# Kernel tuning notes

Measured on AMD Instinct MI355X. Metric: run time of the kernel, lower is better.

## Reference

```python
import jax, jax.numpy as jnp
import numpy as np

H = 8
D_MODEL = 512
NEG = -1e9  # fp32 masking value from the torch source


def setup_inputs() -> dict:
    key = jax.random.key(0)
    ks = jax.random.split(key, 13)
    B, T, C, D = 2, 512, 8, D_MODEL
    s = 1.0 / np.sqrt(D)
    inp = {
        "query": jax.random.normal(ks[0], (B, T, C, D), jnp.float32),
        "key": jax.random.normal(ks[1], (B, T, C, D), jnp.float32),
        "value": jax.random.normal(ks[2], (B, T, C, D), jnp.float32),
        "mask": jax.random.randint(ks[3], (B, T, T, 1), 0, 2, jnp.int32),
        # four Linear(d_model, d_model) layers, stored as (in, out)
        "Wq": jax.random.normal(ks[4], (D, D), jnp.float32) * s,
        "bq": jax.random.normal(ks[5], (D,), jnp.float32) * s,
        "Wk": jax.random.normal(ks[6], (D, D), jnp.float32) * s,
        "bk": jax.random.normal(ks[7], (D,), jnp.float32) * s,
        "Wv": jax.random.normal(ks[8], (D, D), jnp.float32) * s,
        "bv": jax.random.normal(ks[9], (D,), jnp.float32) * s,
        "Wo": jax.random.normal(ks[10], (D, D), jnp.float32) * s,
        "bo": jax.random.normal(ks[11], (D,), jnp.float32) * s,
    }
    return inp


def _mha(query, key, value, mask, Wq, bq, Wk, bk, Wv, bv, Wo, bo):
    B, T, C, D = query.shape
    h, dk = H, D // H

    def proj(x, W, b):
        y = (x @ W + b).reshape(B, T, C, h, dk)
        return jnp.transpose(y, (0, 3, 2, 1, 4))  # [B,h,C,T,dk] (torch transpose(1,3))

    q = proj(query, Wq, bq)
    k = proj(key, Wk, bk)
    v = proj(value, Wv, bv)

    scores = jnp.einsum("bhctd,bhcsd->bhcts", q, k) / np.sqrt(dk)  # [B,h,C,T,T]
    # The torch view/transpose/view dance is just a permutation putting C last;
    # it is equivalent to masking scores[b,h,c,t,s] where mask[b,t,s,0]==0
    # (mask broadcast over heads h and channels c).
    m = mask[:, :, :, 0]  # [B,T,Tk]
    scores = jnp.where(m[:, None, None, :, :] == 0, NEG, scores)
    p_attn = jax.nn.softmax(scores, axis=-1)
    # dropout omitted (inference/deterministic reference)
    x = jnp.einsum("bhcts,bhcsd->bhctd", p_attn, v)  # [B,h,C,T,dk]
    x = jnp.transpose(x, (0, 3, 2, 1, 4)).reshape(B, T, C, D)
    return x @ Wo + bo


def reference(query, key, value, mask, Wq, bq, Wk, bk, Wv, bv, Wo, bo):
    return _mha(query, key, value, mask, Wq, bq, Wk, bk, Wv, bv, Wo, bo)
```

## Files before the change

kernel.cpp:

```cpp
#include <hip/hip_runtime.h>
#include <hip/hip_bf16.h>

typedef __bf16 bf16;
typedef __bf16 bf16x8 __attribute__((ext_vector_type(8)));
typedef float floatx4 __attribute__((ext_vector_type(4)));


#define AS1 __attribute__((address_space(1)))
#define AS3 __attribute__((address_space(3)))

__device__ __forceinline__ void gload_lds16(const bf16* g, bf16* l) {
    __builtin_amdgcn_global_load_lds((const AS1 unsigned int*)g,
                                     (AS3 unsigned int*)l, 16, 0, 0);
}

union Pack8 { bf16 h[8]; uint4 u; };

__global__ __launch_bounds__(256) void wtr_kernel(
    const float* __restrict__ Wq, const float* __restrict__ Wk,
    const float* __restrict__ Wv, const float* __restrict__ Wo,
    bf16* __restrict__ WT)
{
    __shared__ float Ts[64][65];
    const int tid = threadIdx.x;
    const int k0 = blockIdx.x * 64;
    const int n0 = blockIdx.y * 64;
    const int z  = blockIdx.z;
    const float* W = (z == 0) ? Wq : (z == 1) ? Wk : (z == 2) ? Wv : Wo;
    bf16* O = WT + (size_t)z * 512 * 512;
    #pragma unroll
    for (int i = 0; i < 16; i++) {
        const int r = i * 4 + (tid >> 6), c = tid & 63;
        Ts[r][c] = W[(size_t)(k0 + r) * 512 + n0 + c];
    }
    __syncthreads();
    #pragma unroll
    for (int i = 0; i < 16; i++) {
        const int a = i * 4 + (tid >> 6), c = tid & 63;
        O[(size_t)(n0 + a) * 512 + k0 + c] = (bf16)Ts[c][a];
    }
}

__global__ __launch_bounds__(256) void gemm_qkv(
    const float* __restrict__ Aq, const float* __restrict__ Ak,
    const float* __restrict__ Av, const bf16* __restrict__ WT,
    const float* __restrict__ Bq, const float* __restrict__ Bk,
    const float* __restrict__ Bv,
    bf16* __restrict__ Oq, bf16* __restrict__ Ok, bf16* __restrict__ Ov)
{
    __shared__ bf16 Asm[128 * 32];
    __shared__ bf16 Bsm[128 * 32];
    const int z = blockIdx.z;
    const float* A    = (z == 0) ? Aq : (z == 1) ? Ak : Av;
    const float* bias = (z == 0) ? Bq : (z == 1) ? Bk : Bv;
    bf16* out         = (z == 0) ? Oq : (z == 1) ? Ok : Ov;
    const bf16* BT = WT + (size_t)z * 262144;
    const float scale = (z == 0) ? 0.125f : 1.0f;

    const int tid  = threadIdx.x;
    const int lane = tid & 63;
    const int wave = tid >> 6;
    const int quad = lane >> 4;
    const int l16  = lane & 15;
    const int mblk = blockIdx.x * 128;
    const int nblk = blockIdx.y * 128;

    const int srow = wave * 16 + (lane >> 2);
    const int scol = (lane & 3) * 8;
    const float* Ag0 = A + (size_t)(mblk + srow) * 512 + scol;
    const float* Ag1 = Ag0 + (size_t)64 * 512;
    const bf16* Bg0 = BT + (size_t)(nblk + srow) * 512 + scol;
    const bf16* Bg1 = Bg0 + (size_t)64 * 512;
    bf16* Alp0 = Asm + srow * 32 + scol;
    bf16* Alp1 = Alp0 + 64 * 32;
    bf16* Bl0 = Bsm + wave * 16 * 32;
    bf16* Bl1 = Bsm + (64 + wave * 16) * 32;

    const int wr = (wave >> 1) * 64;
    const int wc = (wave & 1) * 64;

    floatx4 acc[4][4] = {};
    for (int k0 = 0; k0 < 512; k0 += 32) {
        gload_lds16(Bg0 + k0, Bl0);
        gload_lds16(Bg1 + k0, Bl1);
        float4 x0 = *(const float4*)(Ag0 + k0);
        float4 x1 = *(const float4*)(Ag0 + k0 + 4);
        float4 y0 = *(const float4*)(Ag1 + k0);
        float4 y1 = *(const float4*)(Ag1 + k0 + 4);
        Pack8 pa, pb;
        pa.h[0] = (bf16)x0.x; pa.h[1] = (bf16)x0.y;
        pa.h[2] = (bf16)x0.z; pa.h[3] = (bf16)x0.w;
        pa.h[4] = (bf16)x1.x; pa.h[5] = (bf16)x1.y;
        pa.h[6] = (bf16)x1.z; pa.h[7] = (bf16)x1.w;
        pb.h[0] = (bf16)y0.x; pb.h[1] = (bf16)y0.y;
        pb.h[2] = (bf16)y0.z; pb.h[3] = (bf16)y0.w;
        pb.h[4] = (bf16)y1.x; pb.h[5] = (bf16)y1.y;
        pb.h[6] = (bf16)y1.z; pb.h[7] = (bf16)y1.w;
        *(uint4*)Alp0 = pa.u;
        *(uint4*)Alp1 = pb.u;
        __syncthreads();
        bf16x8 a[4], b[4];
        #pragma unroll
        for (int mt = 0; mt < 4; mt++)
            a[mt] = *(const bf16x8*)(Asm + (wr + mt * 16 + l16) * 32 + quad * 8);
        #pragma unroll
        for (int nt = 0; nt < 4; nt++)
            b[nt] = *(const bf16x8*)(Bsm + (wc + nt * 16 + l16) * 32 + quad * 8);
        #pragma unroll
        for (int mt = 0; mt < 4; mt++)
            #pragma unroll
            for (int nt = 0; nt < 4; nt++)
                acc[mt][nt] = __builtin_amdgcn_mfma_f32_16x16x32_bf16(
                    a[mt], b[nt], acc[mt][nt], 0, 0, 0);
        __syncthreads();
    }

    #pragma unroll
    for (int mt = 0; mt < 4; mt++) {
        #pragma unroll
        for (int nt = 0; nt < 4; nt++) {
            const int colg = nblk + wc + nt * 16 + l16;
            const float bb = bias[colg];
            #pragma unroll
            for (int r = 0; r < 4; r++) {
                const int rowg = mblk + wr + mt * 16 + quad * 4 + r;
                const float v = (acc[mt][nt][r] + bb) * scale;
                const int b_ = rowg >> 12;
                const int t = (rowg >> 3) & 511;
                const int c = rowg & 7;
                const int h = colg >> 6;
                const int d = colg & 63;
                const int hd = b_ * 64 + h * 8 + c;
                const size_t addr = (z == 2)
                    ? ((size_t)hd * 64 + d) * 512 + t
                    : ((size_t)hd * 512 + t) * 64 + d;
                out[addr] = (bf16)v;
            }
        }
    }
}

template<int LAYOUT, typename TO>
__global__ __launch_bounds__(256) void gemm_bt(
    const bf16* __restrict__ A, const bf16* __restrict__ BT,
    const float* __restrict__ bias, TO* __restrict__ out)
{
    __shared__ bf16 Asm[128 * 32];
    __shared__ bf16 Bsm[128 * 32];
    const int tid  = threadIdx.x;
    const int lane = tid & 63;
    const int wave = tid >> 6;
    const int quad = lane >> 4;
    const int l16  = lane & 15;
    const int mblk = blockIdx.x * 128;
    const int nblk = blockIdx.y * 128;

    const int srow = wave * 16 + (lane >> 2);
    const int scol = (lane & 3) * 8;
    const bf16* Ag0 = A + (size_t)(mblk + srow) * 512 + scol;
    const bf16* Ag1 = Ag0 + (size_t)64 * 512;
    const bf16* Bg0 = BT + (size_t)(nblk + srow) * 512 + scol;
    const bf16* Bg1 = Bg0 + (size_t)64 * 512;
    bf16* Al0 = Asm + wave * 16 * 32;
    bf16* Al1 = Asm + (64 + wave * 16) * 32;
    bf16* Bl0 = Bsm + wave * 16 * 32;
    bf16* Bl1 = Bsm + (64 + wave * 16) * 32;

    const int wr = (wave >> 1) * 64;
    const int wc = (wave & 1) * 64;

    floatx4 acc[4][4] = {};
    for (int k0 = 0; k0 < 512; k0 += 32) {
        gload_lds16(Ag0 + k0, Al0);
        gload_lds16(Ag1 + k0, Al1);
        gload_lds16(Bg0 + k0, Bl0);
        gload_lds16(Bg1 + k0, Bl1);
        __syncthreads();
        bf16x8 a[4], b[4];
        #pragma unroll
        for (int mt = 0; mt < 4; mt++)
            a[mt] = *(const bf16x8*)(Asm + (wr + mt * 16 + l16) * 32 + quad * 8);
        #pragma unroll
        for (int nt = 0; nt < 4; nt++)
            b[nt] = *(const bf16x8*)(Bsm + (wc + nt * 16 + l16) * 32 + quad * 8);
        #pragma unroll
        for (int mt = 0; mt < 4; mt++)
            #pragma unroll
            for (int nt = 0; nt < 4; nt++)
                acc[mt][nt] = __builtin_amdgcn_mfma_f32_16x16x32_bf16(
                    a[mt], b[nt], acc[mt][nt], 0, 0, 0);
        __syncthreads();
    }

    #pragma unroll
    for (int mt = 0; mt < 4; mt++) {
        #pragma unroll
        for (int nt = 0; nt < 4; nt++) {
            const int colg = nblk + wc + nt * 16 + l16;
            const float bb = bias[colg];
            #pragma unroll
            for (int r = 0; r < 4; r++) {
                const int rowg = mblk + wr + mt * 16 + quad * 4 + r;
                const float v = acc[mt][nt][r] + bb;
                if (LAYOUT == 2) {
                    out[(size_t)rowg * 512 + colg] = (TO)v;
                } else {
                    const int b_ = rowg >> 12;
                    const int t = (rowg >> 3) & 511;
                    const int c = rowg & 7;
                    const int h = colg >> 6;
                    const int d = colg & 63;
                    const int hd = b_ * 64 + h * 8 + c;
                    const size_t addr = (LAYOUT == 0)
                        ? ((size_t)hd * 512 + t) * 64 + d
                        : ((size_t)hd * 64 + d) * 512 + t;
                    out[addr] = (TO)v;
                }
            }
        }
    }
}

#define PST 520

__global__ __launch_bounds__(256, 8) void attn_kernel(
    const bf16* __restrict__ Qws, const bf16* __restrict__ Kws,
    const bf16* __restrict__ Vtws, const int* __restrict__ mask,
    bf16* __restrict__ Xws)
{
    __shared__ bf16 MPsm[16][PST];
    __shared__ float redM[4][16];
    __shared__ float redS[4][16];
    const int tid  = threadIdx.x;
    const int wave = tid >> 6;
    const int lane = tid & 63;
    const int quad = lane >> 4;
    const int l16  = lane & 15;
    const int s_ = blockIdx.x;
    const int o_ = ((s_ & 7) << 9) | (s_ >> 3);
    const int qt = o_ & 31;
    const int hd = o_ >> 5;
    const int q0 = qt * 16;
    const int b = hd >> 6;
    const int h = (hd >> 3) & 7;
    const int c = hd & 7;

    {
        const int* mp = mask + ((size_t)b * 512 + q0) * 512;
        #pragma unroll
        for (int it = 0; it < 8; it++) {
            const int idx = (it * 256 + tid) * 4;
            const int4 mv = *(const int4*)(mp + idx);
            const int row = idx >> 9, col = idx & 511;
            union { bf16 h[4]; unsigned long long u; } pk;
            pk.h[0] = (mv.x == 0) ? (bf16)(-1.0e9f) : (bf16)0.0f;
            pk.h[1] = (mv.y == 0) ? (bf16)(-1.0e9f) : (bf16)0.0f;
            pk.h[2] = (mv.z == 0) ? (bf16)(-1.0e9f) : (bf16)0.0f;
            pk.h[3] = (mv.w == 0) ? (bf16)(-1.0e9f) : (bf16)0.0f;
            *(unsigned long long*)&MPsm[row][col] = pk.u;
        }
    }

    const bf16* Qh = Qws + (size_t)hd * 512 * 64;
    const bf16* Kh = Kws + (size_t)hd * 512 * 64;
    bf16x8 aq0 = *(const bf16x8*)(Qh + (size_t)(q0 + l16) * 64 + quad * 8);
    bf16x8 aq1 = *(const bf16x8*)(Qh + (size_t)(q0 + l16) * 64 + 32 + quad * 8);
    __syncthreads();

    float sv[8][4];
    float mx[4] = {-3.0e38f, -3.0e38f, -3.0e38f, -3.0e38f};
    #pragma unroll
    for (int nt = 0; nt < 8; nt++) {
        const int s0 = wave * 128 + nt * 16;
        bf16x8 bk0 = *(const bf16x8*)(Kh + (size_t)(s0 + l16) * 64 + quad * 8);
        bf16x8 bk1 = *(const bf16x8*)(Kh + (size_t)(s0 + l16) * 64 + 32 + quad * 8);
        floatx4 s = {};
        s = __builtin_amdgcn_mfma_f32_16x16x32_bf16(aq0, bk0, s, 0, 0, 0);
        s = __builtin_amdgcn_mfma_f32_16x16x32_bf16(aq1, bk1, s, 0, 0, 0);
        #pragma unroll
        for (int r = 0; r < 4; r++) {
            const float v = s[r] + (float)MPsm[quad * 4 + r][s0 + l16];
            sv[nt][r] = v;
            mx[r] = fmaxf(mx[r], v);
        }
    }
    #pragma unroll
    for (int off = 1; off < 16; off <<= 1)
        #pragma unroll
        for (int r = 0; r < 4; r++)
            mx[r] = fmaxf(mx[r], __shfl_xor(mx[r], off, 64));
    if (l16 == 0)
        #pragma unroll
        for (int r = 0; r < 4; r++) redM[wave][quad * 4 + r] = mx[r];
    __syncthreads();
    float mf[4], sum[4] = {0.f, 0.f, 0.f, 0.f};
    #pragma unroll
    for (int r = 0; r < 4; r++) {
        const int qr = quad * 4 + r;
        mf[r] = fmaxf(fmaxf(redM[0][qr], redM[1][qr]),
                      fmaxf(redM[2][qr], redM[3][qr]));
    }
    #pragma unroll
    for (int nt = 0; nt < 8; nt++)
        #pragma unroll
        for (int r = 0; r < 4; r++) {
            const float e = __expf(sv[nt][r] - mf[r]);
            sv[nt][r] = e;
            sum[r] += e;
        }
    #pragma unroll
    for (int off = 1; off < 16; off <<= 1)
        #pragma unroll
        for (int r = 0; r < 4; r++)
            sum[r] += __shfl_xor(sum[r], off, 64);
    if (l16 == 0)
        #pragma unroll
        for (int r = 0; r < 4; r++) redS[wave][quad * 4 + r] = sum[r];
    __syncthreads();
    float inv[4];
    #pragma unroll
    for (int r = 0; r < 4; r++) {
        const int qr = quad * 4 + r;
        inv[r] = 1.f / (redS[0][qr] + redS[1][qr] + redS[2][qr] + redS[3][qr]);
    }
    #pragma unroll
    for (int nt = 0; nt < 8; nt++)
        #pragma unroll
        for (int r = 0; r < 4; r++)
            MPsm[quad * 4 + r][wave * 128 + nt * 16 + l16] =
                (bf16)(sv[nt][r] * inv[r]);
    __syncthreads();

    const bf16* Vh = Vtws + (size_t)hd * 64 * 512;
    const int d0 = wave * 16;
    floatx4 oacc = {};
    #pragma unroll
    for (int ks = 0; ks < 16; ks++) {
        bf16x8 ap = *(const bf16x8*)(&MPsm[l16][ks * 32 + quad * 8]);
        bf16x8 bv = *(const bf16x8*)(Vh + (size_t)(d0 + l16) * 512 + ks * 32 + quad * 8);
        oacc = __builtin_amdgcn_mfma_f32_16x16x32_bf16(ap, bv, oacc, 0, 0, 0);
    }
    #pragma unroll
    for (int r = 0; r < 4; r++) {
        const int q = quad * 4 + r;
        const size_t row = ((size_t)b * 512 + q0 + q) * 8 + c;
        Xws[row * 512 + h * 64 + d0 + l16] = (bf16)oacc[r];
    }
}

extern "C" void kernel_launch(void* const* d_in, const int* in_sizes, int n_in,
                              void* d_out, int out_size, void* d_ws, size_t ws_size,
                              hipStream_t stream)
{
    const float* qin  = (const float*)d_in[0];
    const float* kin  = (const float*)d_in[1];
    const float* vin  = (const float*)d_in[2];
    const int*   mask = (const int*)d_in[3];
    const float* Bq = (const float*)d_in[5];
    const float* Bk = (const float*)d_in[7];
    const float* Bv = (const float*)d_in[9];
    const float* Bo = (const float*)d_in[11];
    float* out = (float*)d_out;

    const size_t R = (size_t)8192 * 512;
    bf16* r0 = (bf16*)d_ws;
    bf16* r1 = r0 + R;
    bf16* r2 = r1 + R;
    bf16* r3 = r2 + R;
    bf16* WT = r3 + R;

    wtr_kernel<<<dim3(8, 8, 4), dim3(256), 0, stream>>>(
        (const float*)d_in[4], (const float*)d_in[6],
        (const float*)d_in[8], (const float*)d_in[10], WT);
    gemm_qkv<<<dim3(64, 4, 3), dim3(256), 0, stream>>>(
        qin, kin, vin, WT, Bq, Bk, Bv, r0, r1, r2);
    attn_kernel<<<dim3(4096), dim3(256), 0, stream>>>(
        r0, r1, r2, mask, r3);
    gemm_bt<2, float><<<dim3(64, 4), dim3(256), 0, stream>>>(
        r3, WT + (size_t)3 * 262144, Bo, out);
}
```

Baseline: 232.8 us.

## Double-buffer GEMMs with smaller M tiles and read mask directly in attention

Both projection GEMMs move to 64x128 tiles with twice as many blocks and double-buffered LDS. The next K-slice is prefetched while the current one runs through MFMA, and occupancy hints are added. The attention kernel stops building a bf16 mask tile in shared memory and its extra barrier, and instead reads int mask values from global memory inside the score loop. This aims to hide load latency and fill the GPU better, at the cost of more scattered global mask reads and fewer MFMAs per LDS load.

```diff
diff --git a/kernel.cpp b/kernel.cpp
--- a/kernel.cpp
+++ b/kernel.cpp
@@ -41,15 +41,15 @@
     }
 }
 
-__global__ __launch_bounds__(256) void gemm_qkv(
+__global__ __launch_bounds__(256, 4) void gemm_qkv(
     const float* __restrict__ Aq, const float* __restrict__ Ak,
     const float* __restrict__ Av, const bf16* __restrict__ WT,
     const float* __restrict__ Bq, const float* __restrict__ Bk,
     const float* __restrict__ Bv,
     bf16* __restrict__ Oq, bf16* __restrict__ Ok, bf16* __restrict__ Ov)
 {
-    __shared__ bf16 Asm[128 * 32];
-    __shared__ bf16 Bsm[128 * 32];
+    __shared__ bf16 Asm[2][64 * 32];
+    __shared__ bf16 Bsm[2][128 * 32];
     const int z = blockIdx.z;
     const float* A    = (z == 0) ? Aq : (z == 1) ? Ak : Av;
     const float* bias = (z == 0) ? Bq : (z == 1) ? Bk : Bv;
@@ -62,61 +62,74 @@
     const int wave = tid >> 6;
     const int quad = lane >> 4;
     const int l16  = lane & 15;
-    const int mblk = blockIdx.x * 128;
+    const int mblk = blockIdx.x * 64;
     const int nblk = blockIdx.y * 128;
 
     const int srow = wave * 16 + (lane >> 2);
     const int scol = (lane & 3) * 8;
-    const float* Ag0 = A + (size_t)(mblk + srow) * 512 + scol;
-    const float* Ag1 = Ag0 + (size_t)64 * 512;
+    const float* Ag = A + (size_t)(mblk + srow) * 512 + scol;
     const bf16* Bg0 = BT + (size_t)(nblk + srow) * 512 + scol;
     const bf16* Bg1 = Bg0 + (size_t)64 * 512;
-    bf16* Alp0 = Asm + srow * 32 + scol;
-    bf16* Alp1 = Alp0 + 64 * 32;
-    bf16* Bl0 = Bsm + wave * 16 * 32;
-    bf16* Bl1 = Bsm + (64 + wave * 16) * 32;
-
-    const int wr = (wave >> 1) * 64;
+    const int aoff  = srow * 32 + scol;
+    const int b0off = wave * 16 * 32;
+    const int b1off = (64 + wave * 16) * 32;
+
+    const int wr = (wave >> 1) * 32;
     const int wc = (wave & 1) * 64;
 
-    floatx4 acc[4][4] = {};
-    for (int k0 = 0; k0 < 512; k0 += 32) {
-        gload_lds16(Bg0 + k0, Bl0);
-        gload_lds16(Bg1 + k0, Bl1);
-        float4 x0 = *(const float4*)(Ag0 + k0);
-        float4 x1 = *(const float4*)(Ag0 + k0 + 4);
-        float4 y0 = *(const float4*)(Ag1 + k0);
-        float4 y1 = *(const float4*)(Ag1 + k0 + 4);
-        Pack8 pa, pb;
+    floatx4 acc[2][4] = {};
+
+    {
+        gload_lds16(Bg0, Bsm[0] + b0off);
+        gload_lds16(Bg1, Bsm[0] + b1off);
+        float4 x0 = *(const float4*)(Ag);
+        float4 x1 = *(const float4*)(Ag + 4);
+        Pack8 pa;
         pa.h[0] = (bf16)x0.x; pa.h[1] = (bf16)x0.y;
         pa.h[2] = (bf16)x0.z; pa.h[3] = (bf16)x0.w;
         pa.h[4] = (bf16)x1.x; pa.h[5] = (bf16)x1.y;
         pa.h[6] = (bf16)x1.z; pa.h[7] = (bf16)x1.w;
-        pb.h[0] = (bf16)y0.x; pb.h[1] = (bf16)y0.y;
-        pb.h[2] = (bf16)y0.z; pb.h[3] = (bf16)y0.w;
-        pb.h[4] = (bf16)y1.x; pb.h[5] = (bf16)y1.y;
-        pb.h[6] = (bf16)y1.z; pb.h[7] = (bf16)y1.w;
-        *(uint4*)Alp0 = pa.u;
-        *(uint4*)Alp1 = pb.u;
+        *(uint4*)(Asm[0] + aoff) = pa.u;
         __syncthreads();
-        bf16x8 a[4], b[4];
-        #pragma unroll
-        for (int mt = 0; mt < 4; mt++)
-            a[mt] = *(const bf16x8*)(Asm + (wr + mt * 16 + l16) * 32 + quad * 8);
+    }
+
+    #pragma unroll 2
+    for (int t = 0; t < 16; t++) {
+        const int cur = t & 1;
+        float4 x0, x1;
+        if (t < 15) {
+            const int k1 = (t + 1) * 32;
+            gload_lds16(Bg0 + k1, Bsm[cur ^ 1] + b0off);
+            gload_lds16(Bg1 + k1, Bsm[cur ^ 1] + b1off);
+            x0 = *(const float4*)(Ag + k1);
+            x1 = *(const float4*)(Ag + k1 + 4);
+        }
+        bf16x8 a[2], b[4];
+        #pragma unroll
+        for (int mt = 0; mt < 2; mt++)
+            a[mt] = *(const bf16x8*)(Asm[cur] + (wr + mt * 16 + l16) * 32 + quad * 8);
         #pragma unroll
         for (int nt = 0; nt < 4; nt++)
-            b[nt] = *(const bf16x8*)(Bsm + (wc + nt * 16 + l16) * 32 + quad * 8);
-        #pragma unroll
-        for (int mt = 0; mt < 4; mt++)
+            b[nt] = *(const bf16x8*)(Bsm[cur] + (wc + nt * 16 + l16) * 32 + quad * 8);
+        #pragma unroll
+        for (int mt = 0; mt < 2; mt++)
             #pragma unroll
             for (int nt = 0; nt < 4; nt++)
                 acc[mt][nt] = __builtin_amdgcn_mfma_f32_16x16x32_bf16(
                     a[mt], b[nt], acc[mt][nt], 0, 0, 0);
+        if (t < 15) {
+            Pack8 pa;
+            pa.h[0] = (bf16)x0.x; pa.h[1] = (bf16)x0.y;
+            pa.h[2] = (bf16)x0.z; pa.h[3] = (bf16)x0.w;
+            pa.h[4] = (bf16)x1.x; pa.h[5] = (bf16)x1.y;
+            pa.h[6] = (bf16)x1.z; pa.h[7] = (bf16)x1.w;
+            *(uint4*)(Asm[cur ^ 1] + aoff) = pa.u;
+        }
         __syncthreads();
     }
 
     #pragma unroll
-    for (int mt = 0; mt < 4; mt++) {
+    for (int mt = 0; mt < 2; mt++) {
         #pragma unroll
         for (int nt = 0; nt < 4; nt++) {
             const int colg = nblk + wc + nt * 16 + l16;
@@ -126,65 +139,71 @@
                 const int rowg = mblk + wr + mt * 16 + quad * 4 + r;
                 const float v = (acc[mt][nt][r] + bb) * scale;
                 const int b_ = rowg >> 12;
-                const int t = (rowg >> 3) & 511;
-                const int c = rowg & 7;
-                const int h = colg >> 6;
-                const int d = colg & 63;
+                const int t_ = (rowg >> 3) & 511;
+                const int c  = rowg & 7;
+                const int h  = colg >> 6;
+                const int d  = colg & 63;
                 const int hd = b_ * 64 + h * 8 + c;
                 const size_t addr = (z == 2)
-                    ? ((size_t)hd * 64 + d) * 512 + t
-                    : ((size_t)hd * 512 + t) * 64 + d;
+                    ? ((size_t)hd * 64 + d) * 512 + t_
+                    : ((size_t)hd * 512 + t_) * 64 + d;
                 out[addr] = (bf16)v;
             }
         }
     }
 }
 
-template<int LAYOUT, typename TO>
-__global__ __launch_bounds__(256) void gemm_bt(
+__global__ __launch_bounds__(256, 6) void gemm_o(
     const bf16* __restrict__ A, const bf16* __restrict__ BT,
-    const float* __restrict__ bias, TO* __restrict__ out)
-{
-    __shared__ bf16 Asm[128 * 32];
-    __shared__ bf16 Bsm[128 * 32];
+    const float* __restrict__ bias, float* __restrict__ out)
+{
+    __shared__ bf16 Asm[2][64 * 32];
+    __shared__ bf16 Bsm[2][128 * 32];
     const int tid  = threadIdx.x;
     const int lane = tid & 63;
     const int wave = tid >> 6;
     const int quad = lane >> 4;
     const int l16  = lane & 15;
-    const int mblk = blockIdx.x * 128;
+    const int mblk = blockIdx.x * 64;
     const int nblk = blockIdx.y * 128;
 
     const int srow = wave * 16 + (lane >> 2);
     const int scol = (lane & 3) * 8;
-    const bf16* Ag0 = A + (size_t)(mblk + srow) * 512 + scol;
-    const bf16* Ag1 = Ag0 + (size_t)64 * 512;
+    const bf16* Ag  = A + (size_t)(mblk + srow) * 512 + scol;
     const bf16* Bg0 = BT + (size_t)(nblk + srow) * 512 + scol;
     const bf16* Bg1 = Bg0 + (size_t)64 * 512;
-    bf16* Al0 = Asm + wave * 16 * 32;
-    bf16* Al1 = Asm + (64 + wave * 16) * 32;
-    bf16* Bl0 = Bsm + wave * 16 * 32;
-    bf16* Bl1 = Bsm + (64 + wave * 16) * 32;
-
-    const int wr = (wave >> 1) * 64;
+    const int a0off = wave * 16 * 32;
+    const int b0off = wave * 16 * 32;
+    const int b1off = (64 + wave * 16) * 32;
+
+    const int wr = (wave >> 1) * 32;
     const int wc = (wave & 1) * 64;
 
-    floatx4 acc[4][4] = {};
-    for (int k0 = 0; k0 < 512; k0 += 32) {
-        gload_lds16(Ag0 + k0, Al0);
-        gload_lds16(Ag1 + k0, Al1);
-        gload_lds16(Bg0 + k0, Bl0);
-        gload_lds16(Bg1 + k0, Bl1);
-        __syncthreads();
-        bf16x8 a[4], b[4];
-        #pragma unroll
-        for (int mt = 0; mt < 4; mt++)
-            a[mt] = *(const bf16x8*)(Asm + (wr + mt * 16 + l16) * 32 + quad * 8);
+    floatx4 acc[2][4] = {};
+
+    gload_lds16(Ag,  Asm[0] + a0off);
+    gload_lds16(Bg0, Bsm[0] + b0off);
+    gload_lds16(Bg1, Bsm[0] + b1off);
+    __syncthreads();
+
+    #pragma unroll 2
+    for (int t = 0; t < 16; t++) {
+        const int cur = t & 1;
+        if (t < 15) {
+            const int k1 = (t + 1) * 32;
+            gload_lds16(Ag + k1,  Asm[cur ^ 1] + a0off);
+            gload_lds16(Bg0 + k1, Bsm[cur ^ 1] + b0off);
+            gload_lds16(Bg1 + k1, Bsm[cur ^ 1] + b1off);
+        }
+        bf16x8 a[2], b[4];
+        #pragma unroll
+        for (int mt = 0; mt < 2; mt++)
+            a[mt] = *(const bf16x8*)(Asm[cur] + (wr + mt * 16 + l16) * 32 + quad * 8);
         #pragma unroll
         for (int nt = 0; nt < 4; nt++)
-            b[nt] = *(const bf16x8*)(Bsm + (wc + nt * 16 + l16) * 32 + quad * 8);
-        #pragma unroll
-        for (int mt = 0; mt < 4; mt++)
+            b[nt] = *(const bf16x8*)(Bsm[cur] + (wc + nt * 16 + l16) * 32 + quad * 8);
+        #pragma unroll
+        for (int mt = 0; mt < 2; mt++)
             #pragma unroll
             for (int nt = 0; nt < 4; nt++)
                 acc[mt][nt] = __builtin_amdgcn_mfma_f32_16x16x32_bf16(
@@ -193,7 +212,7 @@
     }
 
     #pragma unroll
-    for (int mt = 0; mt < 4; mt++) {
+    for (int mt = 0; mt < 2; mt++) {
         #pragma unroll
         for (int nt = 0; nt < 4; nt++) {
             const int colg = nblk + wc + nt * 16 + l16;
@@ -201,21 +220,7 @@
             #pragma unroll
             for (int r = 0; r < 4; r++) {
                 const int rowg = mblk + wr + mt * 16 + quad * 4 + r;
-                const float v = acc[mt][nt][r] + bb;
-                if (LAYOUT == 2) {
-                    out[(size_t)rowg * 512 + colg] = (TO)v;
-                } else {
-                    const int b_ = rowg >> 12;
-                    const int t = (rowg >> 3) & 511;
-                    const int c = rowg & 7;
-                    const int h = colg >> 6;
-                    const int d = colg & 63;
-                    const int hd = b_ * 64 + h * 8 + c;
-                    const size_t addr = (LAYOUT == 0)
-                        ? ((size_t)hd * 512 + t) * 64 + d
-                        : ((size_t)hd * 64 + d) * 512 + t;
-                    out[addr] = (TO)v;
-                }
+                out[(size_t)rowg * 512 + colg] = acc[mt][nt][r] + bb;
             }
         }
     }
@@ -228,7 +233,7 @@
     const bf16* __restrict__ Vtws, const int* __restrict__ mask,
     bf16* __restrict__ Xws)
 {
-    __shared__ bf16 MPsm[16][PST];
+    __shared__ bf16 Psm[16][PST];
     __shared__ float redM[4][16];
     __shared__ float redS[4][16];
     const int tid  = threadIdx.x;
@@ -245,27 +250,11 @@
     const int h = (hd >> 3) & 7;
     const int c = hd & 7;
 
-    {
-        const int* mp = mask + ((size_t)b * 512 + q0) * 512;
-        #pragma unroll
-        for (int it = 0; it < 8; it++) {
-            const int idx = (it * 256 + tid) * 4;
-            const int4 mv = *(const int4*)(mp + idx);
-            const int row = idx >> 9, col = idx & 511;
-            union { bf16 h[4]; unsigned long long u; } pk;
-            pk.h[0] = (mv.x == 0) ? (bf16)(-1.0e9f) : (bf16)0.0f;
-            pk.h[1] = (mv.y == 0) ? (bf16)(-1.0e9f) : (bf16)0.0f;
-            pk.h[2] = (mv.z == 0) ? (bf16)(-1.0e9f) : (bf16)0.0f;
-            pk.h[3] = (mv.w == 0) ? (bf16)(-1.0e9f) : (bf16)0.0f;
-            *(unsigned long long*)&MPsm[row][col] = pk.u;
-        }
-    }
-
+    const int* mp = mask + ((size_t)b * 512 + q0) * 512;
     const bf16* Qh = Qws + (size_t)hd * 512 * 64;
     const bf16* Kh = Kws + (size_t)hd * 512 * 64;
     bf16x8 aq0 = *(const bf16x8*)(Qh + (size_t)(q0 + l16) * 64 + quad * 8);
     bf16x8 aq1 = *(const bf16x8*)(Qh + (size_t)(q0 + l16) * 64 + 32 + quad * 8);
-    __syncthreads();
 
     float sv[8][4];
     float mx[4] = {-3.0e38f, -3.0e38f, -3.0e38f, -3.0e38f};
@@ -279,7 +268,8 @@
         s = __builtin_amdgcn_mfma_f32_16x16x32_bf16(aq1, bk1, s, 0, 0, 0);
         #pragma unroll
         for (int r = 0; r < 4; r++) {
-            const float v = s[r] + (float)MPsm[quad * 4 + r][s0 + l16];
+            const int mv = mp[(size_t)(quad * 4 + r) * 512 + s0 + l16];
+            const float v = s[r] + ((mv == 0) ? -1.0e9f : 0.0f);
             sv[nt][r] = v;
             mx[r] = fmaxf(mx[r], v);
         }
@@ -327,7 +317,7 @@
     for (int nt = 0; nt < 8; nt++)
         #pragma unroll
         for (int r = 0; r < 4; r++)
-            MPsm[quad * 4 + r][wave * 128 + nt * 16 + l16] =
+            Psm[quad * 4 + r][wave * 128 + nt * 16 + l16] =
                 (bf16)(sv[nt][r] * inv[r]);
     __syncthreads();
 
@@ -336,7 +326,7 @@
     floatx4 oacc = {};
     #pragma unroll
     for (int ks = 0; ks < 16; ks++) {
-        bf16x8 ap = *(const bf16x8*)(&MPsm[l16][ks * 32 + quad * 8]);
+        bf16x8 ap = *(const bf16x8*)(&Psm[l16][ks * 32 + quad * 8]);
         bf16x8 bv = *(const bf16x8*)(Vh + (size_t)(d0 + l16) * 512 + ks * 32 + quad * 8);
         oacc = __builtin_amdgcn_mfma_f32_16x16x32_bf16(ap, bv, oacc, 0, 0, 0);
     }
@@ -372,10 +362,10 @@
     wtr_kernel<<<dim3(8, 8, 4), dim3(256), 0, stream>>>(
         (const float*)d_in[4], (const float*)d_in[6],
         (const float*)d_in[8], (const float*)d_in[10], WT);
-    gemm_qkv<<<dim3(64, 4, 3), dim3(256), 0, stream>>>(
+    gemm_qkv<<<dim3(128, 4, 3), dim3(256), 0, stream>>>(
         qin, kin, vin, WT, Bq, Bk, Bv, r0, r1, r2);
     attn_kernel<<<dim3(4096), dim3(256), 0, stream>>>(
         r0, r1, r2, mask, r3);
-    gemm_bt<2, float><<<dim3(64, 4), dim3(256), 0, stream>>>(
+    gemm_o<<<dim3(128, 4), dim3(256), 0, stream>>>(
         r3, WT + (size_t)3 * 262144, Bo, out);
 }
```

Measured after the change: 242.0 us. 1.04x slower.
